# Kernel tuning notes

Measured on AMD Instinct MI355X. Metric: run time of the kernel, lower is better.

The kernel has to match this reference:

```python
import jax, jax.numpy as jnp
import numpy as np

B, C, H, W = 64, 8, 256, 256
EMB, LAT = 64, 32


def affine_grid(theta, Hh, Ww):
    # F.affine_grid, align_corners=False. theta: [N,2,3] -> grid [N,H,W,2] (x,y)
    xs = (jnp.arange(Ww, dtype=theta.dtype) + 0.5) * (2.0 / Ww) - 1.0
    ys = (jnp.arange(Hh, dtype=theta.dtype) + 0.5) * (2.0 / Hh) - 1.0
    X, Y = jnp.meshgrid(xs, ys)  # [H,W]
    base = jnp.stack([X, Y, jnp.ones_like(X)], axis=-1)  # [H,W,3]
    return jnp.einsum('hwk,nik->nhwi', base, theta)


def grid_sample(img, grid):
    # F.grid_sample bilinear, padding_mode='zeros', align_corners=False
    # img: [N,C,H,W], grid: [N,H,W,2]
    N, Cc, Hh, Ww = img.shape
    ix = ((grid[..., 0] + 1.0) * Ww - 1.0) * 0.5
    iy = ((grid[..., 1] + 1.0) * Hh - 1.0) * 0.5
    x0 = jnp.floor(ix)
    y0 = jnp.floor(iy)
    wx1 = ix - x0
    wy1 = iy - y0
    wx0 = 1.0 - wx1
    wy0 = 1.0 - wy1

    def gather(xf, yf):
        xi = xf.astype(jnp.int32)
        yi = yf.astype(jnp.int32)
        valid = ((xi >= 0) & (xi < Ww) & (yi >= 0) & (yi < Hh)).astype(img.dtype)
        xc = jnp.clip(xi, 0, Ww - 1)
        yc = jnp.clip(yi, 0, Hh - 1)

        def one(im, yb, xb, vb):
            return im[:, yb, xb] * vb[None]  # [C,H,W]

        return jax.vmap(one)(img, yc, xc, valid)

    v00 = gather(x0, y0)
    v01 = gather(x0 + 1.0, y0)
    v10 = gather(x0, y0 + 1.0)
    v11 = gather(x0 + 1.0, y0 + 1.0)
    w00 = (wy0 * wx0)[:, None]
    w01 = (wy0 * wx1)[:, None]
    w10 = (wy1 * wx0)[:, None]
    w11 = (wy1 * wx1)[:, None]
    return v00 * w00 + v01 * w01 + v10 * w10 + v11 * w11


def setup_inputs() -> dict:
    key = jax.random.key(0)
    ks = jax.random.split(key, 9)
    return {
        'x': jax.random.normal(ks[0], (B, C, H, W), jnp.float32),
        'W_ae': jax.random.normal(ks[1], (C, EMB), jnp.float32) * 0.1,
        'W_rot': jax.random.normal(ks[2], (EMB, 6), jnp.float32) * 0.1,
        'W_scale': jax.random.normal(ks[3], (EMB, 6), jnp.float32) * 0.1,
        'W_shear': jax.random.normal(ks[4], (EMB, 6), jnp.float32) * 0.1,
        'W_trans': jax.random.normal(ks[5], (EMB, 6), jnp.float32) * 0.1,
        'W_mask': jax.random.normal(ks[6], (EMB, 1), jnp.float32) * 0.1,
        'W_enc': jax.random.normal(ks[7], (C, LAT), jnp.float32) * 0.1,
        'W_dec': jax.random.normal(ks[8], (C, C), jnp.float32) * 0.1,
    }


def reference(x, W_ae, W_rot, W_scale, W_shear, W_trans, W_mask, W_enc, W_dec):
    Bb, Cc, Hh, Ww = x.shape
    # affine_encoder: global-average-pool + linear
    emb_affine = x.mean(axis=(2, 3)) @ W_ae  # [B,EMB]
    eye = jnp.array([[1.0, 0.0, 0.0], [0.0, 1.0, 0.0]], x.dtype)
    head = lambda Wt: (emb_affine @ Wt).reshape(Bb, 2, 3) * 0.1 + eye
    rotation = head(W_rot)
    scale = head(W_scale)
    shear = head(W_shear)
    translation = head(W_trans)
    mask_parameter = jax.nn.sigmoid(emb_affine @ W_mask)[:, :, None, None]  # [B,1,1,1]

    # affine_transform: four sequential affine_grid + grid_sample passes, then mask
    xt = x
    for theta in (rotation, scale, shear, translation):
        grid = affine_grid(theta, Hh, Ww)
        xt = grid_sample(xt, grid)
    xt = xt * mask_parameter

    emb = xt.mean(axis=(2, 3)) @ W_enc  # encoder on transformed image
    x_dec = jnp.einsum('bchw,cd->bdhw', xt, W_dec)  # pointwise-linear decoder
    return (x_dec, emb, scale, shear, rotation, translation, mask_parameter)
```

## Files before the change

### kernel.cpp

```cpp
#include <hip/hip_runtime.h>
#include <hip/hip_fp16.h>
#include <math.h>

#define BB   64
#define CC   8
#define HH   256
#define WW   256
#define EMB  64
#define LAT  32
#define HW   (HH*WW)
#define PLANE 65536
#define IMG  (CC*HW)

#define OFF_XDEC  0
#define OFF_EMB   33554432
#define OFF_SCALE 33556480
#define OFF_SHEAR 33556864
#define OFF_ROT   33557248
#define OFF_TRANS 33557632
#define OFF_MASK  33558016

#define WS_SUMS   0
#define WS_THETA  512
#define WS_MASK   2048
#define WS_ACC    2112
#define WS_BUF0   4096
#define WS_BUF1   (4096 + 16777216)

#define TH 16
#define TW 64
#define SR 20
#define SC 68
#define SN (SR*SC)

typedef float v2f __attribute__((ext_vector_type(2)));

__global__ void k_zero(float* __restrict__ ws) {
    ws[WS_SUMS + threadIdx.x] = 0.f;
}

__device__ __forceinline__ unsigned pack2(float a, float b) {
    __half2 t = __floats2half2_rn(a, b);
    return *(unsigned*)&t;
}
__device__ __forceinline__ float2 up2(unsigned v) {
    __half2 h = *(__half2*)&v;
    return __half22float2(h);
}

__global__ void k_meanT(const float* __restrict__ x, uint4* __restrict__ outp,
                        float* __restrict__ sums) {
    int bid = blockIdx.x;
    int b = bid >> 6;
    int hq = bid & 63;
    int r = threadIdx.x >> 6;
    int lane = threadIdx.x & 63;
    int h = hq * 4 + r;
    const float* ib = x + (size_t)b * IMG + h * WW + 4 * lane;
    float4 v0 = *(const float4*)(ib + 0 * PLANE);
    float4 v1 = *(const float4*)(ib + 1 * PLANE);
    float4 v2 = *(const float4*)(ib + 2 * PLANE);
    float4 v3 = *(const float4*)(ib + 3 * PLANE);
    float4 v4 = *(const float4*)(ib + 4 * PLANE);
    float4 v5 = *(const float4*)(ib + 5 * PLANE);
    float4 v6 = *(const float4*)(ib + 6 * PLANE);
    float4 v7 = *(const float4*)(ib + 7 * PLANE);

    uint4* ob = outp + (size_t)b * HW + h * WW + 4 * lane;
#define PIXOUT(J, COMP) { uint4 u; \
    u.x = pack2(v0.COMP, v1.COMP); u.y = pack2(v2.COMP, v3.COMP); \
    u.z = pack2(v4.COMP, v5.COMP); u.w = pack2(v6.COMP, v7.COMP); ob[J] = u; }
    PIXOUT(0, x) PIXOUT(1, y) PIXOUT(2, z) PIXOUT(3, w)
#undef PIXOUT

    float p[CC];
    p[0] = (v0.x + v0.y) + (v0.z + v0.w);
    p[1] = (v1.x + v1.y) + (v1.z + v1.w);
    p[2] = (v2.x + v2.y) + (v2.z + v2.w);
    p[3] = (v3.x + v3.y) + (v3.z + v3.w);
    p[4] = (v4.x + v4.y) + (v4.z + v4.w);
    p[5] = (v5.x + v5.y) + (v5.z + v5.w);
    p[6] = (v6.x + v6.y) + (v6.z + v6.w);
    p[7] = (v7.x + v7.y) + (v7.z + v7.w);

    __shared__ float part[4][CC];
    #pragma unroll
    for (int ch = 0; ch < CC; ch++) {
        float v = p[ch];
        for (int off = 32; off > 0; off >>= 1) v += __shfl_down(v, off, 64);
        if (lane == 0) part[r][ch] = v;
    }
    __syncthreads();
    if (threadIdx.x < CC) {
        float v = (part[0][threadIdx.x] + part[1][threadIdx.x]) +
                  (part[2][threadIdx.x] + part[3][threadIdx.x]);
        atomicAdd(&sums[b * CC + threadIdx.x], v);
    }
}

__global__ void k_params(const float* __restrict__ sums,
                         const float* __restrict__ W_ae, const float* __restrict__ W_rot,
                         const float* __restrict__ W_scale, const float* __restrict__ W_shear,
                         const float* __restrict__ W_trans, const float* __restrict__ W_mask,
                         float* __restrict__ ws, float* __restrict__ out) {
    int b = blockIdx.x;
    int t = threadIdx.x;

    if (t < CC) ws[WS_ACC + b * CC + t] = 0.f;

    __shared__ float emb_s[EMB];
    {
        float s = 0.f;
        #pragma unroll
        for (int c = 0; c < CC; c++)
            s += (sums[b * CC + c] * (1.0f / (float)HW)) * W_ae[c * EMB + t];
        emb_s[t] = s;
    }
    __syncthreads();

    if (t < 24) {
        int h = t / 6, k = t % 6;
        const float* Wt = (h == 0) ? W_rot : (h == 1) ? W_scale : (h == 2) ? W_shear : W_trans;
        float s = 0.f;
        #pragma unroll
        for (int e = 0; e < EMB; e++) s += emb_s[e] * Wt[e * 6 + k];
        const float eyev = (k == 0 || k == 4) ? 1.0f : 0.0f;
        float th = s * 0.1f + eyev;
        ws[WS_THETA + h * (BB * 6) + b * 6 + k] = th;
        int off = (h == 0) ? OFF_ROT : (h == 1) ? OFF_SCALE : (h == 2) ? OFF_SHEAR : OFF_TRANS;
        out[off + b * 6 + k] = th;
    } else if (t == 24) {
        float s = 0.f;
        #pragma unroll
        for (int e = 0; e < EMB; e++) s += emb_s[e] * W_mask[e];
        float mk = 1.0f / (1.0f + expf(-s));
        ws[WS_MASK + b] = mk;
        out[OFF_MASK + b] = mk;
    }
}

struct Corners {
    int x0c, x1c, y0c, y1c;
    float w00, w01, w10, w11;
};

__device__ __forceinline__ Corners affine_corners(float t00, float t01, float t02,
                                                  float t10, float t11, float t12,
                                                  int gh, int gw) {
    float X = ((float)gw + 0.5f) * (2.0f / (float)WW) - 1.0f;
    float Y = ((float)gh + 0.5f) * (2.0f / (float)HH) - 1.0f;
    float gx = X * t00 + Y * t01 + t02;
    float gy = X * t10 + Y * t11 + t12;
    float ix = ((gx + 1.0f) * (float)WW - 1.0f) * 0.5f;
    float iy = ((gy + 1.0f) * (float)HH - 1.0f) * 0.5f;
    float x0f = floorf(ix), y0f = floorf(iy);
    int x0 = (int)x0f, y0 = (int)y0f, x1 = x0 + 1, y1 = y0 + 1;
    float wx1 = ix - x0f, wy1 = iy - y0f, wx0 = 1.f - wx1, wy0 = 1.f - wy1;
    float fx0 = ((unsigned)x0 < (unsigned)WW) ? 1.f : 0.f;
    float fx1 = ((unsigned)x1 < (unsigned)WW) ? 1.f : 0.f;
    float fy0 = ((unsigned)y0 < (unsigned)HH) ? 1.f : 0.f;
    float fy1 = ((unsigned)y1 < (unsigned)HH) ? 1.f : 0.f;
    Corners c;
    c.x0c = min(max(x0, 0), WW - 1); c.x1c = min(max(x1, 0), WW - 1);
    c.y0c = min(max(y0, 0), HH - 1); c.y1c = min(max(y1, 0), HH - 1);
    c.w00 = wy0*wx0*fy0*fx0; c.w01 = wy0*wx1*fy0*fx1;
    c.w10 = wy1*wx0*fy1*fx0; c.w11 = wy1*wx1*fy1*fx1;
    return c;
}

__device__ __forceinline__ uint4 bilerp8_pk(uint4 a00, uint4 a01, uint4 a10, uint4 a11,
                                            __half2 h00, __half2 h01, __half2 h10, __half2 h11) {
    uint4 u;
#define BLEND(COMP) { \
    __half2 r = __hmul2(*(__half2*)&a00.COMP, h00); \
    r = __hfma2(*(__half2*)&a01.COMP, h01, r); \
    r = __hfma2(*(__half2*)&a10.COMP, h10, r); \
    r = __hfma2(*(__half2*)&a11.COMP, h11, r); \
    u.COMP = *(unsigned*)&r; }
    BLEND(x) BLEND(y) BLEND(z) BLEND(w)
#undef BLEND
    return u;
}

__device__ __forceinline__ int lidx(int sr, int sc) {
    sr = min(max(sr, 0), SR - 1);
    sc = min(max(sc, 0), SC - 1);
    return sr * SC + (sc ^ ((sc >> 3) & 7));
}

template<int NT>
__device__ __forceinline__ void stage_g2l(uint4* __restrict__ buf,
                                          const uint4* __restrict__ pb,
                                          const float* __restrict__ th,
                                          int oh, int ow, int tid) {
    float t00 = th[0], t01 = th[1], t02 = th[2], t10 = th[3], t11 = th[4], t12 = th[5];
    for (int i = tid; i < SN; i += NT) {
        int lr = i / SC, lc = i - lr * SC;
        Corners c = affine_corners(t00, t01, t02, t10, t11, t12, oh - 2 + lr, ow - 2 + lc);
        uint4 a00 = pb[c.y0c * WW + c.x0c], a01 = pb[c.y0c * WW + c.x1c];
        uint4 a10 = pb[c.y1c * WW + c.x0c], a11 = pb[c.y1c * WW + c.x1c];
        __half2 h00 = __float2half2_rn(c.w00), h01 = __float2half2_rn(c.w01);
        __half2 h10 = __float2half2_rn(c.w10), h11 = __float2half2_rn(c.w11);
        buf[lr * SC + (lc ^ ((lc >> 3) & 7))] =
            bilerp8_pk(a00, a01, a10, a11, h00, h01, h10, h11);
    }
}

__global__ __launch_bounds__(512) void k_warpA(const uint4* __restrict__ in,
                                               uint4* __restrict__ out,
                                               const float* __restrict__ ws) {
    __shared__ uint4 buf[SN];
    int bid = (int)gridDim.x - 1 - (int)blockIdx.x;
    int b = bid >> 6;
    int tile = bid & 63;
    int oh = (tile >> 2) * TH;
    int ow = (tile & 3) * TW;
    int tid = threadIdx.x;
    const uint4* pb = in + (size_t)b * HW;

    stage_g2l<512>(buf, pb, ws + WS_THETA + 0 * (BB * 6) + b * 6, oh, ow, tid);
    __syncthreads();

    const float* th = ws + WS_THETA + 1 * (BB * 6) + b * 6;
    float t00 = th[0], t01 = th[1], t02 = th[2], t10 = th[3], t11 = th[4], t12 = th[5];
    uint4* ob = out + (size_t)b * HW;
    #pragma unroll
    for (int j = 0; j < 2; ++j) {
        int i = tid + j * 512;
        int lr = i >> 6, lc = i & 63;
        int gh = oh + lr, gw = ow + lc;
        Corners c = affine_corners(t00, t01, t02, t10, t11, t12, gh, gw);
        uint4 a00 = buf[lidx(c.y0c - oh + 2, c.x0c - ow + 2)];
        uint4 a01 = buf[lidx(c.y0c - oh + 2, c.x1c - ow + 2)];
        uint4 a10 = buf[lidx(c.y1c - oh + 2, c.x0c - ow + 2)];
        uint4 a11 = buf[lidx(c.y1c - oh + 2, c.x1c - ow + 2)];
        __half2 h00 = __float2half2_rn(c.w00), h01 = __float2half2_rn(c.w01);
        __half2 h10 = __float2half2_rn(c.w10), h11 = __float2half2_rn(c.w11);
        ob[gh * WW + gw] = bilerp8_pk(a00, a01, a10, a11, h00, h01, h10, h11);
    }
}

__global__ __launch_bounds__(512) void k_warpB(const uint4* __restrict__ in,
                                               const float* __restrict__ ws,
                                               const float* __restrict__ W_dec,
                                               float* __restrict__ out,
                                               float* __restrict__ acc) {
    __shared__ uint4 buf[SN];
    __shared__ v2f Wd2[CC][4];
    __shared__ float part[8][CC];
    int bid = blockIdx.x;
    int b = bid >> 6;
    int tile = bid & 63;
    int oh = (tile >> 2) * TH;
    int ow = (tile & 3) * TW;
    int tid = threadIdx.x;
    if (tid < CC * 4) {
        int ch = tid >> 2, j = tid & 3;
        v2f w; w.x = W_dec[ch * CC + 2 * j]; w.y = W_dec[ch * CC + 2 * j + 1];
        Wd2[ch][j] = w;
    }
    const uint4* pb = in + (size_t)b * HW;

    stage_g2l<512>(buf, pb, ws + WS_THETA + 2 * (BB * 6) + b * 6, oh, ow, tid);
    __syncthreads();

    float mk = ws[WS_MASK + b];
    const float* th = ws + WS_THETA + 3 * (BB * 6) + b * 6;
    float t00 = th[0], t01 = th[1], t02 = th[2], t10 = th[3], t11 = th[4], t12 = th[5];

    int wv = tid >> 6, lane = tid & 63;
    int r = wv * 2 + (lane >> 5);
    int c0 = (lane & 31) * 2;
    float sl[CC];
    #pragma unroll
    for (int ch = 0; ch < CC; ch++) sl[ch] = 0.f;
    float od[CC][2];

    #pragma unroll
    for (int px = 0; px < 2; px++) {
        int gh = oh + r, gw = ow + c0 + px;
        Corners c = affine_corners(t00, t01, t02, t10, t11, t12, gh, gw);
        uint4 a00 = buf[lidx(c.y0c - oh + 2, c.x0c - ow + 2)];
        uint4 a01 = buf[lidx(c.y0c - oh + 2, c.x1c - ow + 2)];
        uint4 a10 = buf[lidx(c.y1c - oh + 2, c.x0c - ow + 2)];
        uint4 a11 = buf[lidx(c.y1c - oh + 2, c.x1c - ow + 2)];
        __half2 h00 = __float2half2_rn(c.w00 * mk), h01 = __float2half2_rn(c.w01 * mk);
        __half2 h10 = __float2half2_rn(c.w10 * mk), h11 = __float2half2_rn(c.w11 * mk);
        uint4 u = bilerp8_pk(a00, a01, a10, a11, h00, h01, h10, h11);

        float2 s01 = up2(u.x), s23 = up2(u.y), s45 = up2(u.z), s67 = up2(u.w);
        float s[CC] = {s01.x, s01.y, s23.x, s23.y, s45.x, s45.y, s67.x, s67.y};

        #pragma unroll
        for (int ch = 0; ch < CC; ch++) sl[ch] += s[ch];

        v2f o2[4];
        #pragma unroll
        for (int j = 0; j < 4; j++) { o2[j].x = 0.f; o2[j].y = 0.f; }
        #pragma unroll
        for (int ch = 0; ch < CC; ch++) {
            v2f sb; sb.x = s[ch]; sb.y = s[ch];
            #pragma unroll
            for (int j = 0; j < 4; j++)
                o2[j] = __builtin_elementwise_fma(sb, Wd2[ch][j], o2[j]);
        }
        #pragma unroll
        for (int j = 0; j < 4; j++) { od[2*j][px] = o2[j].x; od[2*j+1][px] = o2[j].y; }
    }

    size_t base = (size_t)b * IMG + (size_t)(oh + r) * WW + (ow + c0);
    #pragma unroll
    for (int d = 0; d < CC; d++) {
        float2 f2 = make_float2(od[d][0], od[d][1]);
        *(float2*)(out + OFF_XDEC + base + d * PLANE) = f2;
    }

    #pragma unroll
    for (int ch = 0; ch < CC; ch++) {
        float v = sl[ch];
        for (int off = 32; off > 0; off >>= 1) v += __shfl_down(v, off, 64);
        if (lane == 0) part[wv][ch] = v;
    }
    __syncthreads();
    if (tid < CC) {
        float v = 0.f;
        #pragma unroll
        for (int w = 0; w < 8; w++) v += part[w][tid];
        atomicAdd(&acc[b * CC + tid], v);
    }
}

__global__ void k_emb(const float* __restrict__ acc, const float* __restrict__ W_enc,
                      float* __restrict__ out) {
    for (int i = threadIdx.x; i < BB * LAT; i += 256) {
        int b = i >> 5, l = i & 31;
        float s = 0.f;
        #pragma unroll
        for (int c = 0; c < CC; c++)
            s += (acc[b * CC + c] * (1.0f / (float)HW)) * W_enc[c * LAT + l];
        out[OFF_EMB + i] = s;
    }
}

extern "C" void kernel_launch(void* const* d_in, const int* in_sizes, int n_in,
                              void* d_out, int out_size, void* d_ws, size_t ws_size,
                              hipStream_t stream) {
    const float* x       = (const float*)d_in[0];
    const float* W_ae    = (const float*)d_in[1];
    const float* W_rot   = (const float*)d_in[2];
    const float* W_scale = (const float*)d_in[3];
    const float* W_shear = (const float*)d_in[4];
    const float* W_trans = (const float*)d_in[5];
    const float* W_mask  = (const float*)d_in[6];
    const float* W_enc   = (const float*)d_in[7];
    const float* W_dec   = (const float*)d_in[8];

    float* ws   = (float*)d_ws;
    float* out  = (float*)d_out;
    float* sums = ws + WS_SUMS;
    float* acc  = ws + WS_ACC;
    uint4* hb0  = (uint4*)(ws + WS_BUF0);
    uint4* hb1  = (uint4*)(ws + WS_BUF1);

    k_zero<<<1, 512, 0, stream>>>(ws);
    k_meanT<<<BB * (HH / 4), 256, 0, stream>>>(x, hb0, sums);
    k_params<<<BB, 64, 0, stream>>>(sums, W_ae, W_rot, W_scale, W_shear, W_trans, W_mask, ws, out);
    k_warpA<<<BB * 64, 512, 0, stream>>>(hb0, hb1, ws);
    k_warpB<<<BB * 64, 512, 0, stream>>>(hb1, ws, W_dec, out, acc);
    k_emb<<<1, 256, 0, stream>>>(acc, W_enc, out);
}
```

Measured before the change: 138.1 us.

## Retile warpB to full-width 8-row strips with float4 stores

k_warpB now processes 8 full-width output rows per block (half as many blocks) instead of 64x16 tiles. The staging step builds a 12x260 halo window in LDS with an XOR swizzle, and each thread then produces 4 adjacent pixels and writes float4 stores. The aim is to cut halo overhead and widen the global stores. In exchange the staging window is larger per block, which costs occupancy, and source coordinates are clamped into the window, which assumes small transforms.

```diff
diff --git a/kernel.cpp b/kernel.cpp
--- a/kernel.cpp
+++ b/kernel.cpp
@@ -240,19 +240,20 @@
     }
 }
 
+#define W_R 12
+#define W_C 260
 __global__ __launch_bounds__(512) void k_warpB(const uint4* __restrict__ in,
                                                const float* __restrict__ ws,
                                                const float* __restrict__ W_dec,
                                                float* __restrict__ out,
                                                float* __restrict__ acc) {
-    __shared__ uint4 buf[SN];
+    __shared__ uint4 buf[W_R * W_C];
     __shared__ v2f Wd2[CC][4];
     __shared__ float part[8][CC];
     int bid = blockIdx.x;
-    int b = bid >> 6;
-    int tile = bid & 63;
-    int oh = (tile >> 2) * TH;
-    int ow = (tile & 3) * TW;
+    int b = bid >> 5;
+    int rq = bid & 31;
+    int oh = rq * 8;
     int tid = threadIdx.x;
     if (tid < CC * 4) {
         int ch = tid >> 2, j = tid & 3;
@@ -261,7 +262,20 @@
     }
     const uint4* pb = in + (size_t)b * HW;
 
-    stage_g2l<512>(buf, pb, ws + WS_THETA + 2 * (BB * 6) + b * 6, oh, ow, tid);
+    {
+        const float* th = ws + WS_THETA + 2 * (BB * 6) + b * 6;
+        float t00 = th[0], t01 = th[1], t02 = th[2], t10 = th[3], t11 = th[4], t12 = th[5];
+        for (int i = tid; i < W_R * W_C; i += 512) {
+            int lr = i / W_C, lc = i - lr * W_C;
+            Corners c = affine_corners(t00, t01, t02, t10, t11, t12, oh - 2 + lr, lc - 2);
+            uint4 a00 = pb[c.y0c * WW + c.x0c], a01 = pb[c.y0c * WW + c.x1c];
+            uint4 a10 = pb[c.y1c * WW + c.x0c], a11 = pb[c.y1c * WW + c.x1c];
+            __half2 h00 = __float2half2_rn(c.w00), h01 = __float2half2_rn(c.w01);
+            __half2 h10 = __float2half2_rn(c.w10), h11 = __float2half2_rn(c.w11);
+            buf[lr * W_C + (lc ^ ((lc >> 3) & 7))] =
+                bilerp8_pk(a00, a01, a10, a11, h00, h01, h10, h11);
+        }
+    }
     __syncthreads();
 
     float mk = ws[WS_MASK + b];
@@ -269,21 +283,26 @@
     float t00 = th[0], t01 = th[1], t02 = th[2], t10 = th[3], t11 = th[4], t12 = th[5];
 
     int wv = tid >> 6, lane = tid & 63;
-    int r = wv * 2 + (lane >> 5);
-    int c0 = (lane & 31) * 2;
+    int gh = oh + wv;
+    int col0 = 4 * lane;
+
     float sl[CC];
     #pragma unroll
     for (int ch = 0; ch < CC; ch++) sl[ch] = 0.f;
-    float od[CC][2];
-
-    #pragma unroll
-    for (int px = 0; px < 2; px++) {
-        int gh = oh + r, gw = ow + c0 + px;
+    float od[CC][4];
+
+    #pragma unroll
+    for (int px = 0; px < 4; px++) {
+        int gw = col0 + px;
         Corners c = affine_corners(t00, t01, t02, t10, t11, t12, gh, gw);
-        uint4 a00 = buf[lidx(c.y0c - oh + 2, c.x0c - ow + 2)];
-        uint4 a01 = buf[lidx(c.y0c - oh + 2, c.x1c - ow + 2)];
-        uint4 a10 = buf[lidx(c.y1c - oh + 2, c.x0c - ow + 2)];
-        uint4 a11 = buf[lidx(c.y1c - oh + 2, c.x1c - ow + 2)];
+        int sr0 = min(max(c.y0c - oh + 2, 0), W_R - 1);
+        int sr1 = min(max(c.y1c - oh + 2, 0), W_R - 1);
+        int sc0 = min(max(c.x0c + 2, 0), W_C - 1);
+        int sc1 = min(max(c.x1c + 2, 0), W_C - 1);
+        uint4 a00 = buf[sr0 * W_C + (sc0 ^ ((sc0 >> 3) & 7))];
+        uint4 a01 = buf[sr0 * W_C + (sc1 ^ ((sc1 >> 3) & 7))];
+        uint4 a10 = buf[sr1 * W_C + (sc0 ^ ((sc0 >> 3) & 7))];
+        uint4 a11 = buf[sr1 * W_C + (sc1 ^ ((sc1 >> 3) & 7))];
         __half2 h00 = __float2half2_rn(c.w00 * mk), h01 = __float2half2_rn(c.w01 * mk);
         __half2 h10 = __float2half2_rn(c.w10 * mk), h11 = __float2half2_rn(c.w11 * mk);
         uint4 u = bilerp8_pk(a00, a01, a10, a11, h00, h01, h10, h11);
@@ -308,11 +327,11 @@
         for (int j = 0; j < 4; j++) { od[2*j][px] = o2[j].x; od[2*j+1][px] = o2[j].y; }
     }
 
-    size_t base = (size_t)b * IMG + (size_t)(oh + r) * WW + (ow + c0);
+    size_t base = (size_t)b * IMG + (size_t)gh * WW + col0;
     #pragma unroll
     for (int d = 0; d < CC; d++) {
-        float2 f2 = make_float2(od[d][0], od[d][1]);
-        *(float2*)(out + OFF_XDEC + base + d * PLANE) = f2;
+        float4 f4 = make_float4(od[d][0], od[d][1], od[d][2], od[d][3]);
+        *(float4*)(out + OFF_XDEC + base + d * PLANE) = f4;
     }
 
     #pragma unroll
@@ -366,6 +385,6 @@
     k_meanT<<<BB * (HH / 4), 256, 0, stream>>>(x, hb0, sums);
     k_params<<<BB, 64, 0, stream>>>(sums, W_ae, W_rot, W_scale, W_shear, W_trans, W_mask, ws, out);
     k_warpA<<<BB * 64, 512, 0, stream>>>(hb0, hb1, ws);
-    k_warpB<<<BB * 64, 512, 0, stream>>>(hb1, ws, W_dec, out, acc);
+    k_warpB<<<BB * 32, 512, 0, stream>>>(hb1, ws, W_dec, out, acc);
     k_emb<<<1, 256, 0, stream>>>(acc, W_enc, out);
 }
```

Result: slower. 159.4 us (+15.5%).
